# Kernel tuning notes

Hardware: AMD Instinct MI355X
Metric: run time of the kernel (lower is better)

The kernel has to match this reference:

```python
import jax, jax.numpy as jnp
import numpy as np


def setup_inputs() -> dict:
    key = jax.random.key(0)
    B, T, H, W = 32, 1024, 32, 32
    dim_s = 32
    # spike ids per (batch, time, h, w), values in [0, dim_s)
    inp = jax.random.randint(key, (B, T, H, W), 0, dim_s, dtype=jnp.int32)
    return {"input": inp, "dim_s": dim_s}


def reference(input, dim_s):
    # input: [B, T, H, W] int32 spike ids in [0, dim_s)
    # out:   [B, dim_s, H, W] int32 counts: out[b,s,h,w] = #{t : input[b,t,h,w]==s}
    B, T, H, W = input.shape
    b_idx = jnp.arange(B, dtype=jnp.int32)[:, None, None, None]   # [B,1,1,1]
    h_idx = jnp.arange(H, dtype=jnp.int32)[None, None, :, None]   # [1,1,H,1]
    w_idx = jnp.arange(W, dtype=jnp.int32)[None, None, None, :]   # [1,1,1,W]
    hist = jnp.zeros((B, dim_s, H, W), dtype=jnp.int32)
    # scatter-add one count per (b, t, h, w) into bin input[b,t,h,w]
    hist = hist.at[b_idx, input, h_idx, w_idx].add(jnp.int32(1))
    return hist
```

## Files before the change

### kernel.cpp

```cpp
#include <hip/hip_runtime.h>


constexpr int T_DIM   = 1024;
constexpr int HW      = 1024;
constexpr int DIM_S   = 32;
constexpr int PIX_PB  = 64;
constexpr int TQ      = 8;
constexpr int THREADS = PIX_PB * TQ;
constexpr int T_PER_THREAD = T_DIM / TQ;
constexpr int PLANE_CHUNKS = HW / PIX_PB;
constexpr int NGROUP  = T_PER_THREAD / 32;

__global__ __launch_bounds__(THREADS) void spike_hist_kernel(
    const int* __restrict__ in, int* __restrict__ out) {
    __shared__ int lds[DIM_S][THREADS];

    const int tid  = threadIdx.x;
    const int blk  = blockIdx.x;
    const int b    = blk >> 4;
    const int pix0 = (blk & (PLANE_CHUNKS - 1)) * PIX_PB;
    const int pix  = tid & (PIX_PB - 1);
    const int tq   = tid >> 6;

    const int* __restrict__ p = in
        + (size_t)b * (T_DIM * HW)
        + (size_t)(tq * T_PER_THREAD) * HW
        + pix0 + pix;

    int cnt[DIM_S];
    #pragma unroll
    for (int s = 0; s < DIM_S; ++s) cnt[s] = 0;

    #pragma unroll
    for (int g = 0; g < NGROUP; ++g) {
        unsigned p0 = 0, p1 = 0, p2 = 0, p3 = 0, p4 = 0;
        #pragma unroll
        for (int h = 0; h < 2; ++h) {
            unsigned v[16];
            #pragma unroll
            for (int i = 0; i < 16; ++i)
                v[i] = (unsigned)p[(size_t)(g * 32 + h * 16 + i) * HW];
            #pragma unroll
            for (int i = 0; i < 16; ++i) {
                const int sh = h * 16 + i;
                const unsigned x = v[i];
                p0 |= (x        & 1u) << sh;
                p1 |= ((x >> 1) & 1u) << sh;
                p2 |= ((x >> 2) & 1u) << sh;
                p3 |= ((x >> 3) & 1u) << sh;
                p4 |= ((x >> 4) & 1u) << sh;
            }
        }
        const unsigned n0 = ~p0, n1 = ~p1, n2 = ~p2, n3 = ~p3, n4 = ~p4;
        const unsigned a[4]  = { n1 & n0, n1 & p0, p1 & n0, p1 & p0 };
        const unsigned bq[4] = { n3 & n2, n3 & p2, p3 & n2, p3 & p2 };
        #pragma unroll
        for (int j = 0; j < 4; ++j) {
            #pragma unroll
            for (int k = 0; k < 4; ++k) {
                const unsigned ab = bq[j] & a[k];
                cnt[j * 4 + k]      += __builtin_popcount(ab & n4);
                cnt[16 + j * 4 + k] += __builtin_popcount(ab & p4);
            }
        }
    }

    #pragma unroll
    for (int s = 0; s < DIM_S; ++s) lds[s][tid] = cnt[s];
    __syncthreads();

    int* __restrict__ outb = out + (size_t)b * (DIM_S * HW) + pix0;
    #pragma unroll
    for (int r = 0; r < 4; ++r) {
        const int e    = r * THREADS + tid;
        const int opix = e & (PIX_PB - 1);
        const int s    = e >> 6;
        int sum = 0;
        #pragma unroll
        for (int q = 0; q < TQ; ++q)
            sum += lds[s][q * PIX_PB + opix];
        outb[(size_t)s * HW + opix] = sum;
    }
}

extern "C" void kernel_launch(void* const* d_in, const int* in_sizes, int n_in,
                              void* d_out, int out_size, void* d_ws, size_t ws_size,
                              hipStream_t stream) {
    const int* in = (const int*)d_in[0];
    int* out      = (int*)d_out;
    const int B   = in_sizes[0] / (T_DIM * HW);
    const int grid = B * PLANE_CHUNKS;
    spike_hist_kernel<<<grid, THREADS, 0, stream>>>(in, out);
}
```

Measured before the change: 194.6 us.

## Vectorize loads to int4 per thread and pack byte counters

```diff
diff --git a/kernel.cpp b/kernel.cpp
--- a/kernel.cpp
+++ b/kernel.cpp
@@ -4,82 +4,107 @@
 constexpr int T_DIM   = 1024;
 constexpr int HW      = 1024;
 constexpr int DIM_S   = 32;
-constexpr int PIX_PB  = 64;
-constexpr int TQ      = 8;
-constexpr int THREADS = PIX_PB * TQ;
-constexpr int T_PER_THREAD = T_DIM / TQ;
-constexpr int PLANE_CHUNKS = HW / PIX_PB;
-constexpr int NGROUP  = T_PER_THREAD / 32;
+constexpr int PIX_PB  = 128;
+constexpr int QUADS   = PIX_PB / 4;
+constexpr int THREADS = 512;
+constexpr int SLICES  = THREADS / QUADS;
+constexpr int T_PER_THREAD = T_DIM / SLICES;
+constexpr int CHUNKS  = HW / PIX_PB;
 
 __global__ __launch_bounds__(THREADS) void spike_hist_kernel(
     const int* __restrict__ in, int* __restrict__ out) {
-    __shared__ int lds[DIM_S][THREADS];
+    __shared__ unsigned lds[32 * THREADS];
 
     const int tid  = threadIdx.x;
+    const int quad = tid & (QUADS - 1);
+    const int sl   = tid >> 5;
     const int blk  = blockIdx.x;
-    const int b    = blk >> 4;
-    const int pix0 = (blk & (PLANE_CHUNKS - 1)) * PIX_PB;
-    const int pix  = tid & (PIX_PB - 1);
-    const int tq   = tid >> 6;
+    const int b    = blk >> 3;
+    const int pix0 = (blk & (CHUNKS - 1)) * PIX_PB;
 
-    const int* __restrict__ p = in
+    const int* __restrict__ base = in
         + (size_t)b * (T_DIM * HW)
-        + (size_t)(tq * T_PER_THREAD) * HW
-        + pix0 + pix;
+        + (size_t)(sl * T_PER_THREAD) * HW
+        + pix0 + quad * 4;
 
-    int cnt[DIM_S];
+    unsigned cw[32];
     #pragma unroll
-    for (int s = 0; s < DIM_S; ++s) cnt[s] = 0;
+    for (int m = 0; m < 32; ++m) cw[m] = 0u;
 
     #pragma unroll
-    for (int g = 0; g < NGROUP; ++g) {
-        unsigned p0 = 0, p1 = 0, p2 = 0, p3 = 0, p4 = 0;
+    for (int g = 0; g < 2; ++g) {
+        unsigned pl[4][5];
         #pragma unroll
-        for (int h = 0; h < 2; ++h) {
-            unsigned v[16];
+        for (int c = 0; c < 4; ++c)
             #pragma unroll
-            for (int i = 0; i < 16; ++i)
-                v[i] = (unsigned)p[(size_t)(g * 32 + h * 16 + i) * HW];
+            for (int j = 0; j < 5; ++j) pl[c][j] = 0u;
+
+        #pragma unroll
+        for (int ph = 0; ph < 4; ++ph) {
+            int4 v[8];
             #pragma unroll
-            for (int i = 0; i < 16; ++i) {
-                const int sh = h * 16 + i;
-                const unsigned x = v[i];
-                p0 |= (x        & 1u) << sh;
-                p1 |= ((x >> 1) & 1u) << sh;
-                p2 |= ((x >> 2) & 1u) << sh;
-                p3 |= ((x >> 3) & 1u) << sh;
-                p4 |= ((x >> 4) & 1u) << sh;
+            for (int i = 0; i < 8; ++i)
+                v[i] = *(const int4*)(base + (size_t)(g * 32 + ph * 8 + i) * HW);
+            #pragma unroll
+            for (int i = 0; i < 8; ++i) {
+                const int ti = ph * 8 + i;
+                const unsigned xs[4] = { (unsigned)v[i].x, (unsigned)v[i].y,
+                                         (unsigned)v[i].z, (unsigned)v[i].w };
+                #pragma unroll
+                for (int c = 0; c < 4; ++c) {
+                    const unsigned x = xs[c];
+                    #pragma unroll
+                    for (int j = 0; j < 5; ++j)
+                        pl[c][j] |= ((x >> j) & 1u) << ti;
+                }
             }
         }
-        const unsigned n0 = ~p0, n1 = ~p1, n2 = ~p2, n3 = ~p3, n4 = ~p4;
-        const unsigned a[4]  = { n1 & n0, n1 & p0, p1 & n0, p1 & p0 };
-        const unsigned bq[4] = { n3 & n2, n3 & p2, p3 & n2, p3 & p2 };
+
         #pragma unroll
-        for (int j = 0; j < 4; ++j) {
+        for (int c = 0; c < 4; ++c) {
+            const unsigned p0 = pl[c][0], p1 = pl[c][1], p2 = pl[c][2],
+                           p3 = pl[c][3], p4 = pl[c][4];
+            const unsigned n0 = ~p0, n1 = ~p1, n2 = ~p2, n3 = ~p3, n4 = ~p4;
+            const unsigned a[4]  = { n1 & n0, n1 & p0, p1 & n0, p1 & p0 };
+            const unsigned bq[4] = { n3 & n2, n3 & p2, p3 & n2, p3 & p2 };
             #pragma unroll
-            for (int k = 0; k < 4; ++k) {
-                const unsigned ab = bq[j] & a[k];
-                cnt[j * 4 + k]      += __builtin_popcount(ab & n4);
-                cnt[16 + j * 4 + k] += __builtin_popcount(ab & p4);
+            for (int j = 0; j < 4; ++j) {
+                #pragma unroll
+                for (int k = 0; k < 4; ++k) {
+                    const unsigned ab = bq[j] & a[k];
+                    cw[c * 8 + j]     += (unsigned)__builtin_popcount(ab & n4) << (k * 8);
+                    cw[c * 8 + 4 + j] += (unsigned)__builtin_popcount(ab & p4) << (k * 8);
+                }
             }
         }
     }
 
     #pragma unroll
-    for (int s = 0; s < DIM_S; ++s) lds[s][tid] = cnt[s];
+    for (int m = 0; m < 32; ++m) lds[m * THREADS + tid] = cw[m];
     __syncthreads();
 
     int* __restrict__ outb = out + (size_t)b * (DIM_S * HW) + pix0;
     #pragma unroll
-    for (int r = 0; r < 4; ++r) {
-        const int e    = r * THREADS + tid;
-        const int opix = e & (PIX_PB - 1);
-        const int s    = e >> 6;
-        int sum = 0;
+    for (int k = 0; k < 2; ++k) {
+        const int col = k * THREADS + tid;
+        const int q   = col & 31;
+        const int m   = col >> 5;
+        const int c   = m >> 3;
+        const int w   = m & 7;
+        unsigned lo = 0u, hi = 0u;
         #pragma unroll
-        for (int q = 0; q < TQ; ++q)
-            sum += lds[s][q * PIX_PB + opix];
-        outb[(size_t)s * HW + opix] = sum;
+        for (int s2 = 0; s2 < SLICES; ++s2) {
+            const unsigned x = lds[m * THREADS + s2 * 32 + q];
+            lo += x & 0x00FF00FFu;
+            hi += (x >> 8) & 0x00FF00FFu;
+        }
+        const int s_base = (w >> 2) * 16 + (w & 3) * 4;
+        const int px     = q * 4 + c;
+        int* __restrict__ op = outb + (size_t)s_base * HW + px;
+        op[0 * HW] = (int)(lo & 0xFFFFu);
+        op[1 * HW] = (int)(hi & 0xFFFFu);
+        op[2 * HW] = (int)(lo >> 16);
+        op[3 * HW] = (int)(hi >> 16);
     }
 }
 
@@ -89,6 +114,6 @@
     const int* in = (const int*)d_in[0];
     int* out      = (int*)d_out;
     const int B   = in_sizes[0] / (T_DIM * HW);
-    const int grid = B * PLANE_CHUNKS;
+    const int grid = B * CHUNKS;
     spike_hist_kernel<<<grid, THREADS, 0, stream>>>(in, out);
 }
```

Measured after the change: 192.6 us (median of 2 runs). Within noise of the previous version (-1.0%).
